# Kernel tuning notes

Measured on AMD Instinct MI355X. Metric: run time of the kernel, lower is better.

Reference implementation:

```python
import jax, jax.numpy as jnp
import numpy as np

OUTLINER_RATIO = 0.01
SUB_OUTLINER_BIT = 8


def _get_statistics(x, outliner_ratio, sub_bit):
    # threshold from the first batch element, as in torch.kthvalue(x[0].flatten(), ...)
    flat = jnp.abs(x[0]).ravel()
    k = int(flat.shape[0] * (1.0 - outliner_ratio))  # static python int
    outliner = jnp.sort(flat)[k - 1]
    x_out0 = jnp.where(jnp.abs(x[0]) > outliner, x[0], 0.0)
    x_sub0 = x[0] - x_out0
    qmax = float(2 ** (sub_bit - 1) - 1)
    scale = jnp.max(jnp.abs(x_sub0)) / qmax
    return outliner, scale


def _compress(x, outliner, scale, sub_bit):
    # split into fp outliers + low-bit quantized sub-outlier residual
    x_outlier = jnp.where(jnp.abs(x) > outliner, x, 0.0)
    x_sub = x - x_outlier
    qmin = -(2 ** (sub_bit - 1))
    qmax = 2 ** (sub_bit - 1) - 1
    q = jnp.clip(jnp.round(x_sub / scale), qmin, qmax).astype(jnp.int8)
    return x_outlier, q


def setup_inputs() -> dict:
    key = jax.random.key(0)
    x = jax.random.normal(key, (8, 2048, 4096), dtype=jnp.float32)
    return {"x": x}


def reference(x):
    # forward activation
    result = jax.nn.silu(x)
    # outlier-aware compression statistics (iteration < 10 path)
    outliner, scale = _get_statistics(x, OUTLINER_RATIO, SUB_OUTLINER_BIT)
    x_outlier_compressed, x_sub_q = _compress(x, outliner, scale, SUB_OUTLINER_BIT)
    # module returns (silu(x), outliner, max_norm_column_list, scale); the
    # column list is unused downstream so we return the float outputs
    return (result, outliner, scale)
```

## Files before the change

### kernel.cpp

```cpp
#include <hip/hip_runtime.h>

#define NBINS 4096
#define BPT (NBINS / 256)

struct SelState {
  unsigned prefix;
  unsigned krem;
  unsigned bins[NBINS];
};

__global__ __launch_bounds__(256) void init_state_kernel(SelState* st, unsigned k) {
  int t = threadIdx.x;
  for (int j = t; j < NBINS; j += 256) st->bins[j] = 0u;
  if (t == 0) { st->prefix = 0u; st->krem = k; }
}

__global__ __launch_bounds__(256) void silu_kernel(const float4* __restrict__ x,
                                                   float4* __restrict__ out, int nvec) {
  int i = blockIdx.x * blockDim.x + threadIdx.x;
  int stride = gridDim.x * blockDim.x;
  for (; i < nvec; i += stride) {
    float4 v = x[i];
    float4 r;
    r.x = v.x / (1.0f + __expf(-v.x));
    r.y = v.y / (1.0f + __expf(-v.y));
    r.z = v.z / (1.0f + __expf(-v.z));
    r.w = v.w / (1.0f + __expf(-v.w));
    out[i] = r;
  }
}

__global__ __launch_bounds__(256) void hist_kernel(const uint4* __restrict__ x, int nvec,
                                                   SelState* __restrict__ st,
                                                   unsigned shift, unsigned mask) {
  __shared__ unsigned lbins[NBINS];
  for (int j = threadIdx.x; j < NBINS; j += 256) lbins[j] = 0u;
  __syncthreads();
  unsigned prefix = st->prefix;
  int i = blockIdx.x * blockDim.x + threadIdx.x;
  int stride = gridDim.x * blockDim.x;
  for (; i < nvec; i += stride) {
    uint4 v = x[i];
    unsigned a;
    a = v.x & 0x7fffffffu; if ((a & mask) == prefix) atomicAdd(&lbins[(a >> shift) & (NBINS - 1)], 1u);
    a = v.y & 0x7fffffffu; if ((a & mask) == prefix) atomicAdd(&lbins[(a >> shift) & (NBINS - 1)], 1u);
    a = v.z & 0x7fffffffu; if ((a & mask) == prefix) atomicAdd(&lbins[(a >> shift) & (NBINS - 1)], 1u);
    a = v.w & 0x7fffffffu; if ((a & mask) == prefix) atomicAdd(&lbins[(a >> shift) & (NBINS - 1)], 1u);
  }
  __syncthreads();
  for (int j = threadIdx.x; j < NBINS; j += 256) {
    unsigned c = lbins[j];
    if (c) atomicAdd(&st->bins[j], c);
  }
}

__global__ __launch_bounds__(256) void scan_kernel(SelState* __restrict__ st, unsigned shift,
                                                   float* __restrict__ out_scalars) {
  __shared__ unsigned csum[256];
  const int t = threadIdx.x;
  unsigned local[BPT];
  unsigned s = 0;
  for (int j = 0; j < BPT; ++j) {
    local[j] = st->bins[t * BPT + j];
    s += local[j];
  }
  csum[t] = s;
  __syncthreads();
  for (int off = 1; off < 256; off <<= 1) {
    unsigned add = (t >= off) ? csum[t - off] : 0u;
    __syncthreads();
    csum[t] += add;
    __syncthreads();
  }
  unsigned incl = csum[t];
  unsigned excl = incl - s;
  unsigned krem = st->krem;
  if (krem > excl && krem <= incl) {
    unsigned run = excl;
    unsigned newprefix = st->prefix;
    for (int j = 0; j < BPT; ++j) {
      if (krem <= run + local[j]) {
        unsigned b = (unsigned)(t * BPT + j);
        newprefix |= (b << shift);
        st->prefix = newprefix;
        st->krem = krem - run;
        if (out_scalars) {
          float v = __uint_as_float(newprefix);
          out_scalars[0] = v;
          out_scalars[1] = v / 127.0f;
        }
        break;
      }
      run += local[j];
    }
  }
  __syncthreads();
  for (int j = 0; j < BPT; ++j) st->bins[t * BPT + j] = 0u;
}

extern "C" void kernel_launch(void* const* d_in, const int* in_sizes, int n_in,
                              void* d_out, int out_size, void* d_ws, size_t ws_size,
                              hipStream_t stream) {
  const float* x = (const float*)d_in[0];
  float* out = (float*)d_out;
  const int n = in_sizes[0];
  const int n0 = n / 8;
  const unsigned k = (unsigned)((double)n0 * 0.99);

  SelState* st = (SelState*)d_ws;

  init_state_kernel<<<1, 256, 0, stream>>>(st, k);

  const int nvec0 = n0 / 4;
  dim3 hb(256), hg(2048);
  hist_kernel<<<hg, hb, 0, stream>>>((const uint4*)x, nvec0, st, 19u, 0x00000000u);
  scan_kernel<<<1, 256, 0, stream>>>(st, 19u, nullptr);
  hist_kernel<<<hg, hb, 0, stream>>>((const uint4*)x, nvec0, st, 7u, 0xFFF80000u);
  scan_kernel<<<1, 256, 0, stream>>>(st, 7u, nullptr);
  hist_kernel<<<hg, hb, 0, stream>>>((const uint4*)x, nvec0, st, 0u, 0xFFFFFF80u);
  scan_kernel<<<1, 256, 0, stream>>>(st, 0u, out + n);

  const int nvec = n / 4;
  silu_kernel<<<4096, 256, 0, stream>>>((const float4*)x, (float4*)out, nvec);
}
```

Baseline: 518.5 us.

## Fuse first radix histogram into SiLU pass and compact candidates for selection

The first 12-bit histogram pass over x[0] is merged into the SiLU kernel, so that slice is read only once for both jobs. The two later full radix-select passes over x[0] are replaced by one compaction pass. It gathers the values in the chosen top bin into a candidate buffer, and a single-block kernel resolves the remaining bits from that buffer. SiLU also uses a hardware reciprocal instead of a divide. The risks are LDS atomic contention inside the streaming kernel and fixed candidate capacity limits, per block and global, that assume the chosen bin holds few values.

```diff
diff --git a/kernel.cpp b/kernel.cpp
--- a/kernel.cpp
+++ b/kernel.cpp
@@ -1,69 +1,63 @@
 #include <hip/hip_runtime.h>
 
 #define NBINS 4096
-#define BPT (NBINS / 256)
+#define CAP   (1 << 20)
 
-struct SelState {
-  unsigned prefix;
+struct Ws {
+  unsigned bins[NBINS];
+  unsigned ncand;
+  unsigned b1;
   unsigned krem;
-  unsigned bins[NBINS];
+  unsigned cand[CAP];
 };
 
-__global__ __launch_bounds__(256) void init_state_kernel(SelState* st, unsigned k) {
+__global__ __launch_bounds__(256) void init_kernel(Ws* ws) {
   int t = threadIdx.x;
-  for (int j = t; j < NBINS; j += 256) st->bins[j] = 0u;
-  if (t == 0) { st->prefix = 0u; st->krem = k; }
+  for (int j = t; j < NBINS; j += 256) ws->bins[j] = 0u;
+  if (t == 0) ws->ncand = 0u;
 }
 
-__global__ __launch_bounds__(256) void silu_kernel(const float4* __restrict__ x,
-                                                   float4* __restrict__ out, int nvec) {
+__global__ __launch_bounds__(256) void silu_hist_kernel(const float4* __restrict__ x,
+                                                        float4* __restrict__ out,
+                                                        int nvec, int nvec0,
+                                                        unsigned* __restrict__ gbins) {
+  __shared__ unsigned lbins[NBINS];
+  for (int j = threadIdx.x; j < NBINS; j += 256) lbins[j] = 0u;
+  __syncthreads();
+
   int i = blockIdx.x * blockDim.x + threadIdx.x;
   int stride = gridDim.x * blockDim.x;
   for (; i < nvec; i += stride) {
     float4 v = x[i];
     float4 r;
-    r.x = v.x / (1.0f + __expf(-v.x));
-    r.y = v.y / (1.0f + __expf(-v.y));
-    r.z = v.z / (1.0f + __expf(-v.z));
-    r.w = v.w / (1.0f + __expf(-v.w));
+    r.x = v.x * __builtin_amdgcn_rcpf(1.0f + __expf(-v.x));
+    r.y = v.y * __builtin_amdgcn_rcpf(1.0f + __expf(-v.y));
+    r.z = v.z * __builtin_amdgcn_rcpf(1.0f + __expf(-v.z));
+    r.w = v.w * __builtin_amdgcn_rcpf(1.0f + __expf(-v.w));
     out[i] = r;
-  }
-}
-
-__global__ __launch_bounds__(256) void hist_kernel(const uint4* __restrict__ x, int nvec,
-                                                   SelState* __restrict__ st,
-                                                   unsigned shift, unsigned mask) {
-  __shared__ unsigned lbins[NBINS];
-  for (int j = threadIdx.x; j < NBINS; j += 256) lbins[j] = 0u;
-  __syncthreads();
-  unsigned prefix = st->prefix;
-  int i = blockIdx.x * blockDim.x + threadIdx.x;
-  int stride = gridDim.x * blockDim.x;
-  for (; i < nvec; i += stride) {
-    uint4 v = x[i];
-    unsigned a;
-    a = v.x & 0x7fffffffu; if ((a & mask) == prefix) atomicAdd(&lbins[(a >> shift) & (NBINS - 1)], 1u);
-    a = v.y & 0x7fffffffu; if ((a & mask) == prefix) atomicAdd(&lbins[(a >> shift) & (NBINS - 1)], 1u);
-    a = v.z & 0x7fffffffu; if ((a & mask) == prefix) atomicAdd(&lbins[(a >> shift) & (NBINS - 1)], 1u);
-    a = v.w & 0x7fffffffu; if ((a & mask) == prefix) atomicAdd(&lbins[(a >> shift) & (NBINS - 1)], 1u);
+    if (i < nvec0) {
+      unsigned a;
+      a = __float_as_uint(v.x) & 0x7fffffffu; atomicAdd(&lbins[a >> 19], 1u);
+      a = __float_as_uint(v.y) & 0x7fffffffu; atomicAdd(&lbins[a >> 19], 1u);
+      a = __float_as_uint(v.z) & 0x7fffffffu; atomicAdd(&lbins[a >> 19], 1u);
+      a = __float_as_uint(v.w) & 0x7fffffffu; atomicAdd(&lbins[a >> 19], 1u);
+    }
   }
   __syncthreads();
   for (int j = threadIdx.x; j < NBINS; j += 256) {
     unsigned c = lbins[j];
-    if (c) atomicAdd(&st->bins[j], c);
+    if (c) atomicAdd(&gbins[j], c);
   }
 }
 
-__global__ __launch_bounds__(256) void scan_kernel(SelState* __restrict__ st, unsigned shift,
-                                                   float* __restrict__ out_scalars) {
-  __shared__ unsigned csum[256];
+__device__ inline void select_bin(const unsigned* lbins, int nbins, unsigned krem,
+                                  unsigned* csum, unsigned* sel) {
   const int t = threadIdx.x;
-  unsigned local[BPT];
+  const int per = (nbins + 255) >> 8;
+  const int lo = t * per;
+  const int hi = (lo + per < nbins) ? lo + per : nbins;
   unsigned s = 0;
-  for (int j = 0; j < BPT; ++j) {
-    local[j] = st->bins[t * BPT + j];
-    s += local[j];
-  }
+  for (int j = lo; j < hi; ++j) s += lbins[j];
   csum[t] = s;
   __syncthreads();
   for (int off = 1; off < 256; off <<= 1) {
@@ -72,30 +66,88 @@
     csum[t] += add;
     __syncthreads();
   }
-  unsigned incl = csum[t];
-  unsigned excl = incl - s;
-  unsigned krem = st->krem;
+  unsigned incl = csum[t], excl = incl - s;
   if (krem > excl && krem <= incl) {
     unsigned run = excl;
-    unsigned newprefix = st->prefix;
-    for (int j = 0; j < BPT; ++j) {
-      if (krem <= run + local[j]) {
-        unsigned b = (unsigned)(t * BPT + j);
-        newprefix |= (b << shift);
-        st->prefix = newprefix;
-        st->krem = krem - run;
-        if (out_scalars) {
-          float v = __uint_as_float(newprefix);
-          out_scalars[0] = v;
-          out_scalars[1] = v / 127.0f;
-        }
-        break;
-      }
-      run += local[j];
+    for (int j = lo; j < hi; ++j) {
+      unsigned c = lbins[j];
+      if (krem <= run + c) { sel[0] = (unsigned)j; sel[1] = krem - run; break; }
+      run += c;
     }
   }
   __syncthreads();
-  for (int j = 0; j < BPT; ++j) st->bins[t * BPT + j] = 0u;
+}
+
+__global__ __launch_bounds__(256) void scan1_kernel(Ws* __restrict__ ws, unsigned k) {
+  __shared__ unsigned csum[256];
+  __shared__ unsigned sel[2];
+  select_bin(ws->bins, NBINS, k, csum, sel);
+  if (threadIdx.x == 0) { ws->b1 = sel[0]; ws->krem = sel[1]; }
+}
+
+__global__ __launch_bounds__(256) void compact_kernel(const uint4* __restrict__ x, int nvec0,
+                                                      Ws* __restrict__ ws) {
+  __shared__ unsigned lcand[1024];
+  __shared__ unsigned lcnt, gbase;
+  if (threadIdx.x == 0) lcnt = 0u;
+  __syncthreads();
+  const unsigned b1 = ws->b1;
+  int i = blockIdx.x * blockDim.x + threadIdx.x;
+  int stride = gridDim.x * blockDim.x;
+  for (; i < nvec0; i += stride) {
+    uint4 v = x[i];
+    unsigned a;
+    a = v.x & 0x7fffffffu; if ((a >> 19) == b1) { unsigned p = atomicAdd(&lcnt, 1u); if (p < 1024u) lcand[p] = a; }
+    a = v.y & 0x7fffffffu; if ((a >> 19) == b1) { unsigned p = atomicAdd(&lcnt, 1u); if (p < 1024u) lcand[p] = a; }
+    a = v.z & 0x7fffffffu; if ((a >> 19) == b1) { unsigned p = atomicAdd(&lcnt, 1u); if (p < 1024u) lcand[p] = a; }
+    a = v.w & 0x7fffffffu; if ((a >> 19) == b1) { unsigned p = atomicAdd(&lcnt, 1u); if (p < 1024u) lcand[p] = a; }
+  }
+  __syncthreads();
+  unsigned cnt = lcnt < 1024u ? lcnt : 1024u;
+  if (threadIdx.x == 0 && cnt) gbase = atomicAdd(&ws->ncand, cnt);
+  __syncthreads();
+  for (unsigned j = threadIdx.x; j < cnt; j += 256) {
+    unsigned g = gbase + j;
+    if (g < (unsigned)CAP) ws->cand[g] = lcand[j];
+  }
+}
+
+__global__ __launch_bounds__(256) void final_kernel(Ws* __restrict__ ws,
+                                                    float* __restrict__ out_scalars) {
+  __shared__ unsigned lbins[NBINS];
+  __shared__ unsigned csum[256];
+  __shared__ unsigned sel[2];
+  const int t = threadIdx.x;
+  const unsigned nc = ws->ncand < (unsigned)CAP ? ws->ncand : (unsigned)CAP;
+  const unsigned b1 = ws->b1;
+  unsigned krem = ws->krem;
+
+  for (int j = t; j < NBINS; j += 256) lbins[j] = 0u;
+  __syncthreads();
+  for (unsigned j = t; j < nc; j += 256) {
+    unsigned a = ws->cand[j];
+    atomicAdd(&lbins[(a >> 7) & 0xFFFu], 1u);
+  }
+  __syncthreads();
+  select_bin(lbins, NBINS, krem, csum, sel);
+  const unsigned b2 = sel[0];
+  krem = sel[1];
+  __syncthreads();
+
+  for (int j = t; j < 128; j += 256) lbins[j] = 0u;
+  __syncthreads();
+  for (unsigned j = t; j < nc; j += 256) {
+    unsigned a = ws->cand[j];
+    if (((a >> 7) & 0xFFFu) == b2) atomicAdd(&lbins[a & 0x7Fu], 1u);
+  }
+  __syncthreads();
+  select_bin(lbins, 128, krem, csum, sel);
+  if (t == 0) {
+    unsigned bits = (b1 << 19) | (b2 << 7) | sel[0];
+    float v = __uint_as_float(bits);
+    out_scalars[0] = v;
+    out_scalars[1] = v / 127.0f;
+  }
 }
 
 extern "C" void kernel_launch(void* const* d_in, const int* in_sizes, int n_in,
@@ -107,19 +159,14 @@
   const int n0 = n / 8;
   const unsigned k = (unsigned)((double)n0 * 0.99);
 
-  SelState* st = (SelState*)d_ws;
+  Ws* ws = (Ws*)d_ws;
+  const int nvec = n / 4;
+  const int nvec0 = n0 / 4;
 
-  init_state_kernel<<<1, 256, 0, stream>>>(st, k);
-
-  const int nvec0 = n0 / 4;
-  dim3 hb(256), hg(2048);
-  hist_kernel<<<hg, hb, 0, stream>>>((const uint4*)x, nvec0, st, 19u, 0x00000000u);
-  scan_kernel<<<1, 256, 0, stream>>>(st, 19u, nullptr);
-  hist_kernel<<<hg, hb, 0, stream>>>((const uint4*)x, nvec0, st, 7u, 0xFFF80000u);
-  scan_kernel<<<1, 256, 0, stream>>>(st, 7u, nullptr);
-  hist_kernel<<<hg, hb, 0, stream>>>((const uint4*)x, nvec0, st, 0u, 0xFFFFFF80u);
-  scan_kernel<<<1, 256, 0, stream>>>(st, 0u, out + n);
-
-  const int nvec = n / 4;
-  silu_kernel<<<4096, 256, 0, stream>>>((const float4*)x, (float4*)out, nvec);
+  init_kernel<<<1, 256, 0, stream>>>(ws);
+  silu_hist_kernel<<<8192, 256, 0, stream>>>((const float4*)x, (float4*)out,
+                                             nvec, nvec0, ws->bins);
+  scan1_kernel<<<1, 256, 0, stream>>>(ws, k);
+  compact_kernel<<<2048, 256, 0, stream>>>((const uint4*)x, nvec0, ws);
+  final_kernel<<<1, 256, 0, stream>>>(ws, out + n);
 }
```

Result: slower. 583.6 us (+12.6%).
